# Optimization experiments

Hardware: AMD Instinct MI355X
Metric: run time of the kernel (lower is better)

Reference implementation:

```python
import jax, jax.numpy as jnp
import numpy as np

CHUNK = (10, 10, 10)          # chunk_shape from init_kwargs
VSHAPE = (40, 40, 200)        # spatial shape of each block
GRID_MAX = 1000               # locations drawn from [0, GRID_MAX)
SPAN = 256                    # > (GRID_MAX + max(VSHAPE)) / min(CHUNK); per-dim chunk-grid span for key linearization
NBATCH = 64


def setup_inputs() -> dict:
    key = jax.random.key(0)
    k1, k2 = jax.random.split(key)
    data = jax.random.normal(k1, (NBATCH, *VSHAPE), dtype=jnp.float32)
    location = jax.random.randint(k2, (NBATCH, 3), 0, GRID_MAX, dtype=jnp.int32)
    return {"data": data, "location": location}


def _chunkify(data, location):
    """Rebin each block into chunk-grid-aligned tiles of shape CHUNK.
    data: [B, V0, V1, V2]; location: [B, 3] int offsets in the global grid.
    Returns (chunks [M, *CHUNK], locs [M, 3]) with M = B * prod(nchunks)."""
    B = data.shape[0]
    C = jnp.array(CHUNK, dtype=jnp.int32)
    shift = location % C          # [B,3] offset of block origin within its first chunk
    start = location - shift      # [B,3] chunk-aligned envelope origin
    # Fixed-size envelope V + C per dim covers any shift in [0, C).
    E = tuple(v + c for v, c in zip(VSHAPE, CHUNK))
    nch = tuple(e // c for e, c in zip(E, CHUNK))  # chunks per dim: (5, 5, 21)

    def pad_one(d, sh):
        # padded[j0,j1,j2] = d[j - sh] where in range, else 0 (gather + mask, no scatter)
        idx = [jnp.arange(E[k]) - sh[k] for k in range(3)]
        valid = [(ix >= 0) & (ix < VSHAPE[k]) for k, ix in enumerate(idx)]
        cidx = [jnp.clip(ix, 0, VSHAPE[k] - 1) for k, ix in enumerate(idx)]
        g = d[cidx[0][:, None, None], cidx[1][None, :, None], cidx[2][None, None, :]]
        m = valid[0][:, None, None] & valid[1][None, :, None] & valid[2][None, None, :]
        return jnp.where(m, g, jnp.float32(0))

    padded = jax.vmap(pad_one)(data, shift)  # [B, E0, E1, E2]
    padded = padded.reshape(B, nch[0], CHUNK[0], nch[1], CHUNK[1], nch[2], CHUNK[2])
    chunks = padded.transpose(0, 1, 3, 5, 2, 4, 6).reshape(-1, *CHUNK)
    # per-chunk global locations
    g = jnp.stack(jnp.meshgrid(jnp.arange(nch[0]), jnp.arange(nch[1]),
                               jnp.arange(nch[2]), indexing='ij'), axis=-1)  # [n0,n1,n2,3]
    locs = start[:, None, None, None, :] + g[None].astype(jnp.int32) * C     # [B,n0,n1,n2,3]
    return chunks, locs.reshape(-1, 3)


def _accumulate(chunks, locs):
    """Sum chunks sharing the same global chunk location (scatter-add reduce).
    Output padded to a fixed M rows (jit-friendly); padding rows are zero."""
    M = chunks.shape[0]
    C = jnp.array(CHUNK, dtype=jnp.int32)
    cg = locs // C  # chunk-grid coordinates, each < SPAN
    keys = (cg[:, 0] * SPAN + cg[:, 1]) * SPAN + cg[:, 2]  # int32 linearized key
    ukeys, inv = jnp.unique(keys, return_inverse=True, size=M,
                            fill_value=jnp.int32(2**31 - 1))
    out = jax.ops.segment_sum(chunks.reshape(M, -1), inv, num_segments=M)
    out = out.reshape(M, *CHUNK)
    uloc = jnp.stack([ukeys // (SPAN * SPAN), (ukeys // SPAN) % SPAN,
                      ukeys % SPAN], axis=-1).astype(jnp.int32) * C
    return out, uloc


def reference(data, location):
    chunks, locs = _chunkify(data, location)
    return _accumulate(chunks, locs)
```

## Files before the change

### kernel.cpp

```cpp
#include <hip/hip_runtime.h>
#include <hip/hip_bf16.h>

namespace {
constexpr int NB    = 64;
constexpr int V0d   = 40, V1d = 40, V2d = 200;
constexpr int VOL   = V0d * V1d * V2d;
constexpr int NC0   = 5, NC1 = 5, NC2 = 21;
constexpr int CELLS = NC0 * NC1 * NC2;
constexpr int M     = NB * CELLS;
constexpr int C1MAX = 104, C2MAX = 120;
constexpr int KS    = 104 * C1MAX * C2MAX;
constexpr int SEG   = 4096;
constexpr int NSEG  = (KS + SEG - 1) / SEG;
constexpr int KSP   = NSEG * SEG;
constexpr int CHVOL = 1000;
}

__device__ __forceinline__ float bf16r(float v) {
    return __bfloat162float(__float2bfloat16(v));
}

__device__ __forceinline__ int enc(int c0, int c1, int c2) {
    return (c0 * C1MAX + c1) * C2MAX + c2;
}

__global__ void k_zero(int* __restrict__ P, int4* __restrict__ mask4) {
    int idx = blockIdx.x * blockDim.x + threadIdx.x;
    int stride = gridDim.x * blockDim.x;
    int4* p4 = reinterpret_cast<int4*>(P);
    const int n4 = KSP / 4;
    for (int i = idx; i < n4; i += stride) p4[i] = make_int4(0, 0, 0, 0);
    const int m4 = M * 8 / 16;
    for (int i = idx; i < m4; i += stride) mask4[i] = make_int4(0, 0, 0, 0);
}

__global__ void k_mark(const int* __restrict__ loc, int* __restrict__ P) {
    int m = blockIdx.x * blockDim.x + threadIdx.x;
    if (m >= M) return;
    int b = m / CELLS, cell = m % CELLS;
    int i = cell / (NC1 * NC2), j = (cell / NC2) % NC1, k = cell % NC2;
    P[enc(loc[b * 3 + 0] / 10 + i, loc[b * 3 + 1] / 10 + j,
          loc[b * 3 + 2] / 10 + k)] = 1;
}

__global__ __launch_bounds__(256) void k_scan_blocks(int* __restrict__ P,
                                                     int* __restrict__ Bsums) {
    int bid = blockIdx.x, t = threadIdx.x;
    int4* p4 = reinterpret_cast<int4*>(P + (size_t)bid * SEG + t * 16);
    int4 a = p4[0], b = p4[1], c = p4[2], d = p4[3];
    int v[16] = {a.x, a.y, a.z, a.w, b.x, b.y, b.z, b.w,
                 c.x, c.y, c.z, c.w, d.x, d.y, d.z, d.w};
    int s = 0;
#pragma unroll
    for (int e = 0; e < 16; ++e) s += v[e];
    __shared__ int sc[256];
    sc[t] = s;
    __syncthreads();
#pragma unroll
    for (int off = 1; off < 256; off <<= 1) {
        int x = (t >= off) ? sc[t - off] : 0;
        __syncthreads();
        sc[t] += x;
        __syncthreads();
    }
    int incl = sc[t];
    if (t == 255) Bsums[bid] = incl;
    int run = incl - s;
#pragma unroll
    for (int e = 0; e < 16; ++e) { int x = v[e]; v[e] = run; run += x; }
    p4[0] = make_int4(v[0], v[1], v[2], v[3]);
    p4[1] = make_int4(v[4], v[5], v[6], v[7]);
    p4[2] = make_int4(v[8], v[9], v[10], v[11]);
    p4[3] = make_int4(v[12], v[13], v[14], v[15]);
}

__global__ __launch_bounds__(256) void k_scan_sums(int* __restrict__ Bsums,
                                                   int* __restrict__ U) {
    __shared__ int sc[256];
    __shared__ int carry_s;
    int t = threadIdx.x;
    if (t == 0) carry_s = 0;
    __syncthreads();
    for (int base = 0; base < NSEG; base += 256) {
        int idx = base + t;
        int vv = (idx < NSEG) ? Bsums[idx] : 0;
        sc[t] = vv;
        __syncthreads();
#pragma unroll
        for (int off = 1; off < 256; off <<= 1) {
            int x = (t >= off) ? sc[t - off] : 0;
            __syncthreads();
            sc[t] += x;
            __syncthreads();
        }
        int incl = sc[t];
        int carry = carry_s;
        if (idx < NSEG) Bsums[idx] = carry + incl - vv;
        __syncthreads();
        if (t == 255) carry_s = carry + incl;
        __syncthreads();
    }
    if (t == 0) U[0] = carry_s;
}

__global__ void k_slots(const int* __restrict__ loc, const int* __restrict__ P,
                        const int* __restrict__ Bsums, int* __restrict__ ukeys,
                        unsigned long long* __restrict__ mask) {
    int m = blockIdx.x * blockDim.x + threadIdx.x;
    if (m >= M) return;
    int b = m / CELLS, cell = m % CELLS;
    int i = cell / (NC1 * NC2), j = (cell / NC2) % NC1, k = cell % NC2;
    int d = enc(loc[b * 3 + 0] / 10 + i, loc[b * 3 + 1] / 10 + j,
                loc[b * 3 + 2] / 10 + k);
    int rank = P[d] + Bsums[d / SEG];
    ukeys[rank] = d;
    atomicOr(&mask[rank], 1ull << b);
}

__global__ __launch_bounds__(256) void k_out(const float* __restrict__ data,
                                             const int* __restrict__ loc,
                                             const int* __restrict__ ukeys,
                                             const unsigned long long* __restrict__ mask,
                                             const int* __restrict__ U,
                                             float* __restrict__ out,
                                             long long base_ul) {
    int orig = blockIdx.x;
    int r = (orig & 7) * (M / 8) + (orig >> 3);
    int t = threadIdx.x;

    bool valid = (r < U[0]);
    float ax = 0.f, ay = 0.f, az = 0.f, aw = 0.f;
    int c0 = 0, c1 = 0, c2 = 0;

    if (valid) {
        int d = ukeys[r];
        c0 = d / (C1MAX * C2MAX);
        int rem = d % (C1MAX * C2MAX);
        c1 = rem / C2MAX;
        c2 = rem % C2MAX;
        if (t < 250) {
            int e0 = t * 4;
            int x  = e0 / 100;
            int rm = e0 % 100;
            int y  = rm / 10;
            int z0 = rm % 10;
            int g0 = c0 * 10, g1 = c1 * 10, g2 = c2 * 10;
            unsigned long long mk = mask[r];
            while (mk) {
                int b = __builtin_ctzll(mk);
                mk &= mk - 1;
                int l0 = loc[b * 3 + 0];
                int l1 = loc[b * 3 + 1];
                int l2 = loc[b * 3 + 2];
                const float* db = data + (size_t)b * VOL;
                if (z0 <= 6) {
                    int p0 = g0 - l0 + x, p1 = g1 - l1 + y, p2 = g2 - l2 + z0;
                    if ((unsigned)p0 < (unsigned)V0d &&
                        (unsigned)p1 < (unsigned)V1d) {
                        const float* s = db + (p0 * V1d + p1) * V2d + p2;
                        if (p2 >= 0 && p2 <= V2d - 4) {
                            ax += s[0]; ay += s[1]; az += s[2]; aw += s[3];
                        } else {
                            if ((unsigned)p2       < (unsigned)V2d) ax += s[0];
                            if ((unsigned)(p2 + 1) < (unsigned)V2d) ay += s[1];
                            if ((unsigned)(p2 + 2) < (unsigned)V2d) az += s[2];
                            if ((unsigned)(p2 + 3) < (unsigned)V2d) aw += s[3];
                        }
                    }
                } else {
                    float av[4] = {0.f, 0.f, 0.f, 0.f};
#pragma unroll
                    for (int j = 0; j < 4; ++j) {
                        int e  = e0 + j;
                        int xx = e / 100;
                        int rj = e % 100;
                        int yy = rj / 10, zz = rj % 10;
                        int q0 = g0 - l0 + xx, q1 = g1 - l1 + yy,
                            q2 = g2 - l2 + zz;
                        if ((unsigned)q0 < (unsigned)V0d &&
                            (unsigned)q1 < (unsigned)V1d &&
                            (unsigned)q2 < (unsigned)V2d)
                            av[j] = db[(q0 * V1d + q1) * V2d + q2];
                    }
                    ax += av[0]; ay += av[1]; az += av[2]; aw += av[3];
                }
            }
        }
    }

    if (t < 250) {
        *reinterpret_cast<float4*>(out + (long long)r * CHVOL + t * 4) =
            make_float4(bf16r(ax), bf16r(ay), bf16r(az), bf16r(aw));
    }
    if (t == 0) {
        float u0, u1, u2;
        if (valid) {
            u0 = (float)(c0 * 10);
            u1 = (float)(c1 * 10);
            u2 = (float)(c2 * 10);
        } else {
            u0 = 327670.f; u1 = 2550.f; u2 = 2550.f;
        }
        long long i = base_ul + (long long)r * 3;
        out[i + 0] = bf16r(u0);
        out[i + 1] = bf16r(u1);
        out[i + 2] = bf16r(u2);
    }
}

extern "C" void kernel_launch(void* const* d_in, const int* in_sizes, int n_in,
                              void* d_out, int out_size, void* d_ws, size_t ws_size,
                              hipStream_t stream) {
    const float* data = (const float*)d_in[0];
    const int* loc    = (const int*)d_in[1];
    float* out        = (float*)d_out;

    const size_t bytesP  = (size_t)KSP * 4;
    const size_t bytesSm = (size_t)M * 8
                         + (size_t)(NSEG + 64) * 4
                         + (size_t)M * 4 + 64;
    char* ws = (char*)d_ws;
    int* P;
    char* smalls;
    if (ws_size >= bytesP + bytesSm) {
        P      = (int*)ws;
        smalls = ws + bytesP;
    } else {
        P      = (int*)d_out;
        smalls = ws;
    }
    unsigned long long* mask = (unsigned long long*)smalls;
    int* Bsums = (int*)(smalls + (size_t)M * 8);
    int* ukeys = Bsums + NSEG + 64;
    int* U     = ukeys + M;

    long long out_sz  = (long long)out_size;
    long long base_ul = out_sz - (long long)3 * M;

    k_zero<<<640, 256, 0, stream>>>(P, (int4*)mask);
    k_mark<<<(M + 255) / 256, 256, 0, stream>>>(loc, P);
    k_scan_blocks<<<NSEG, 256, 0, stream>>>(P, Bsums);
    k_scan_sums<<<1, 256, 0, stream>>>(Bsums, U);
    k_slots<<<(M + 255) / 256, 256, 0, stream>>>(loc, P, Bsums, ukeys, mask);
    k_out<<<M, 256, 0, stream>>>(data, loc, ukeys, mask, U, out, base_ul);
}
```

Before: 63.76 us.

## Replace dense int presence array with bitset and popcount-based rank scan

The per-key int presence array (about 1.3M ints) becomes a 32-bit-word bitset marked with atomicOr. The scan now runs over per-word popcounts and ranks are computed with a masked popc, which cuts the zeroing and scan traffic roughly 32x. Validity in the output kernel now comes from a nonzero mask instead of a global unique count, and output stores are nontemporal. The remaining scan is only a few hundred entries, so launch overhead likely dominates those stages.

```diff
diff --git a/kernel.cpp b/kernel.cpp
--- a/kernel.cpp
+++ b/kernel.cpp
@@ -10,11 +10,13 @@
 constexpr int M     = NB * CELLS;
 constexpr int C1MAX = 104, C2MAX = 120;
 constexpr int KS    = 104 * C1MAX * C2MAX;
-constexpr int SEG   = 4096;
-constexpr int NSEG  = (KS + SEG - 1) / SEG;
-constexpr int KSP   = NSEG * SEG;
-constexpr int CHVOL = 1000;
-}
+constexpr int NWORDS = KS / 32;
+constexpr int NSB    = (NWORDS + 255) / 256;
+constexpr int NWPAD  = NSB * 256;
+constexpr int CHVOL  = 1000;
+}
+
+typedef float f32x4 __attribute__((ext_vector_type(4)));
 
 __device__ __forceinline__ float bf16r(float v) {
     return __bfloat162float(__float2bfloat16(v));
@@ -24,118 +26,95 @@
     return (c0 * C1MAX + c1) * C2MAX + c2;
 }
 
-__global__ void k_zero(int* __restrict__ P, int4* __restrict__ mask4) {
+__global__ void k_zero(int4* __restrict__ W4, int4* __restrict__ mask4) {
     int idx = blockIdx.x * blockDim.x + threadIdx.x;
     int stride = gridDim.x * blockDim.x;
-    int4* p4 = reinterpret_cast<int4*>(P);
-    const int n4 = KSP / 4;
-    for (int i = idx; i < n4; i += stride) p4[i] = make_int4(0, 0, 0, 0);
+    const int w4 = NWORDS / 4;
+    for (int i = idx; i < w4; i += stride) W4[i] = make_int4(0, 0, 0, 0);
     const int m4 = M * 8 / 16;
     for (int i = idx; i < m4; i += stride) mask4[i] = make_int4(0, 0, 0, 0);
 }
 
-__global__ void k_mark(const int* __restrict__ loc, int* __restrict__ P) {
-    int m = blockIdx.x * blockDim.x + threadIdx.x;
-    if (m >= M) return;
-    int b = m / CELLS, cell = m % CELLS;
-    int i = cell / (NC1 * NC2), j = (cell / NC2) % NC1, k = cell % NC2;
-    P[enc(loc[b * 3 + 0] / 10 + i, loc[b * 3 + 1] / 10 + j,
-          loc[b * 3 + 2] / 10 + k)] = 1;
-}
-
-__global__ __launch_bounds__(256) void k_scan_blocks(int* __restrict__ P,
-                                                     int* __restrict__ Bsums) {
-    int bid = blockIdx.x, t = threadIdx.x;
-    int4* p4 = reinterpret_cast<int4*>(P + (size_t)bid * SEG + t * 16);
-    int4 a = p4[0], b = p4[1], c = p4[2], d = p4[3];
-    int v[16] = {a.x, a.y, a.z, a.w, b.x, b.y, b.z, b.w,
-                 c.x, c.y, c.z, c.w, d.x, d.y, d.z, d.w};
-    int s = 0;
-#pragma unroll
-    for (int e = 0; e < 16; ++e) s += v[e];
-    __shared__ int sc[256];
-    sc[t] = s;
-    __syncthreads();
-#pragma unroll
-    for (int off = 1; off < 256; off <<= 1) {
-        int x = (t >= off) ? sc[t - off] : 0;
-        __syncthreads();
-        sc[t] += x;
-        __syncthreads();
-    }
-    int incl = sc[t];
-    if (t == 255) Bsums[bid] = incl;
-    int run = incl - s;
-#pragma unroll
-    for (int e = 0; e < 16; ++e) { int x = v[e]; v[e] = run; run += x; }
-    p4[0] = make_int4(v[0], v[1], v[2], v[3]);
-    p4[1] = make_int4(v[4], v[5], v[6], v[7]);
-    p4[2] = make_int4(v[8], v[9], v[10], v[11]);
-    p4[3] = make_int4(v[12], v[13], v[14], v[15]);
-}
-
-__global__ __launch_bounds__(256) void k_scan_sums(int* __restrict__ Bsums,
-                                                   int* __restrict__ U) {
-    __shared__ int sc[256];
-    __shared__ int carry_s;
-    int t = threadIdx.x;
-    if (t == 0) carry_s = 0;
-    __syncthreads();
-    for (int base = 0; base < NSEG; base += 256) {
-        int idx = base + t;
-        int vv = (idx < NSEG) ? Bsums[idx] : 0;
-        sc[t] = vv;
-        __syncthreads();
-#pragma unroll
-        for (int off = 1; off < 256; off <<= 1) {
-            int x = (t >= off) ? sc[t - off] : 0;
-            __syncthreads();
-            sc[t] += x;
-            __syncthreads();
-        }
-        int incl = sc[t];
-        int carry = carry_s;
-        if (idx < NSEG) Bsums[idx] = carry + incl - vv;
-        __syncthreads();
-        if (t == 255) carry_s = carry + incl;
-        __syncthreads();
-    }
-    if (t == 0) U[0] = carry_s;
-}
-
-__global__ void k_slots(const int* __restrict__ loc, const int* __restrict__ P,
-                        const int* __restrict__ Bsums, int* __restrict__ ukeys,
-                        unsigned long long* __restrict__ mask) {
+__global__ void k_mark(const int* __restrict__ loc, unsigned* __restrict__ W) {
     int m = blockIdx.x * blockDim.x + threadIdx.x;
     if (m >= M) return;
     int b = m / CELLS, cell = m % CELLS;
     int i = cell / (NC1 * NC2), j = (cell / NC2) % NC1, k = cell % NC2;
     int d = enc(loc[b * 3 + 0] / 10 + i, loc[b * 3 + 1] / 10 + j,
                 loc[b * 3 + 2] / 10 + k);
-    int rank = P[d] + Bsums[d / SEG];
+    atomicOr(&W[d >> 5], 1u << (d & 31));
+}
+
+__global__ __launch_bounds__(256) void k_scan_words(const unsigned* __restrict__ W,
+                                                    unsigned* __restrict__ WP,
+                                                    int* __restrict__ Bsums) {
+    int t = threadIdx.x;
+    int w = blockIdx.x * 256 + t;
+    int c = (w < NWORDS) ? __popc(W[w]) : 0;
+    __shared__ int sc[256];
+    sc[t] = c;
+    __syncthreads();
+#pragma unroll
+    for (int off = 1; off < 256; off <<= 1) {
+        int x = (t >= off) ? sc[t - off] : 0;
+        __syncthreads();
+        sc[t] += x;
+        __syncthreads();
+    }
+    int incl = sc[t];
+    WP[w] = (unsigned)(incl - c);
+    if (t == 255) Bsums[blockIdx.x] = incl;
+}
+
+__global__ __launch_bounds__(256) void k_scan_sums(int* __restrict__ Bsums) {
+    int t = threadIdx.x;
+    int vv = (t < NSB) ? Bsums[t] : 0;
+    __shared__ int sc[256];
+    sc[t] = vv;
+    __syncthreads();
+#pragma unroll
+    for (int off = 1; off < 256; off <<= 1) {
+        int x = (t >= off) ? sc[t - off] : 0;
+        __syncthreads();
+        sc[t] += x;
+        __syncthreads();
+    }
+    if (t < NSB) Bsums[t] = sc[t] - vv;
+}
+
+__global__ void k_slots(const int* __restrict__ loc, const unsigned* __restrict__ W,
+                        const unsigned* __restrict__ WP, const int* __restrict__ Bsums,
+                        int* __restrict__ ukeys, unsigned long long* __restrict__ mask) {
+    int m = blockIdx.x * blockDim.x + threadIdx.x;
+    if (m >= M) return;
+    int b = m / CELLS, cell = m % CELLS;
+    int i = cell / (NC1 * NC2), j = (cell / NC2) % NC1, k = cell % NC2;
+    int d = enc(loc[b * 3 + 0] / 10 + i, loc[b * 3 + 1] / 10 + j,
+                loc[b * 3 + 2] / 10 + k);
+    int w = d >> 5, bp = d & 31;
+    unsigned wd = W[w];
+    int rank = Bsums[w >> 8] + (int)WP[w] + __popc(wd & ((1u << bp) - 1u));
     ukeys[rank] = d;
     atomicOr(&mask[rank], 1ull << b);
 }
 
 __global__ __launch_bounds__(256) void k_out(const float* __restrict__ data,
-                                             const int* __restrict__ loc,
-                                             const int* __restrict__ ukeys,
-                                             const unsigned long long* __restrict__ mask,
-                                             const int* __restrict__ U,
-                                             float* __restrict__ out,
-                                             long long base_ul) {
+        const int* __restrict__ loc, const int* __restrict__ ukeys,
+        const unsigned long long* __restrict__ mask,
+        float* __restrict__ out, long long base_ul) {
     int orig = blockIdx.x;
     int r = (orig & 7) * (M / 8) + (orig >> 3);
     int t = threadIdx.x;
 
-    bool valid = (r < U[0]);
+    unsigned long long mk = mask[r];
+    int key = ukeys[r];
+    bool valid = (mk != 0ull);
+
     float ax = 0.f, ay = 0.f, az = 0.f, aw = 0.f;
     int c0 = 0, c1 = 0, c2 = 0;
-
     if (valid) {
-        int d = ukeys[r];
-        c0 = d / (C1MAX * C2MAX);
-        int rem = d % (C1MAX * C2MAX);
+        c0 = key / (C1MAX * C2MAX);
+        int rem = key % (C1MAX * C2MAX);
         c1 = rem / C2MAX;
         c2 = rem % C2MAX;
         if (t < 250) {
@@ -145,13 +124,11 @@
             int y  = rm / 10;
             int z0 = rm % 10;
             int g0 = c0 * 10, g1 = c1 * 10, g2 = c2 * 10;
-            unsigned long long mk = mask[r];
-            while (mk) {
-                int b = __builtin_ctzll(mk);
-                mk &= mk - 1;
-                int l0 = loc[b * 3 + 0];
-                int l1 = loc[b * 3 + 1];
-                int l2 = loc[b * 3 + 2];
+            unsigned long long m2 = mk;
+            while (m2) {
+                int b = __builtin_ctzll(m2);
+                m2 &= m2 - 1;
+                int l0 = loc[b * 3 + 0], l1 = loc[b * 3 + 1], l2 = loc[b * 3 + 2];
                 const float* db = data + (size_t)b * VOL;
                 if (z0 <= 6) {
                     int p0 = g0 - l0 + x, p1 = g1 - l1 + y, p2 = g2 - l2 + z0;
@@ -170,8 +147,8 @@
                 } else {
                     float av[4] = {0.f, 0.f, 0.f, 0.f};
 #pragma unroll
-                    for (int j = 0; j < 4; ++j) {
-                        int e  = e0 + j;
+                    for (int jj = 0; jj < 4; ++jj) {
+                        int e  = e0 + jj;
                         int xx = e / 100;
                         int rj = e % 100;
                         int yy = rj / 10, zz = rj % 10;
@@ -180,7 +157,7 @@
                         if ((unsigned)q0 < (unsigned)V0d &&
                             (unsigned)q1 < (unsigned)V1d &&
                             (unsigned)q2 < (unsigned)V2d)
-                            av[j] = db[(q0 * V1d + q1) * V2d + q2];
+                            av[jj] = db[(q0 * V1d + q1) * V2d + q2];
                     }
                     ax += av[0]; ay += av[1]; az += av[2]; aw += av[3];
                 }
@@ -189,8 +166,9 @@
     }
 
     if (t < 250) {
-        *reinterpret_cast<float4*>(out + (long long)r * CHVOL + t * 4) =
-            make_float4(bf16r(ax), bf16r(ay), bf16r(az), bf16r(aw));
+        f32x4 v = {bf16r(ax), bf16r(ay), bf16r(az), bf16r(aw)};
+        __builtin_nontemporal_store(v,
+            reinterpret_cast<f32x4*>(out + (long long)r * CHVOL + t * 4));
     }
     if (t == 0) {
         float u0, u1, u2;
@@ -202,9 +180,9 @@
             u0 = 327670.f; u1 = 2550.f; u2 = 2550.f;
         }
         long long i = base_ul + (long long)r * 3;
-        out[i + 0] = bf16r(u0);
-        out[i + 1] = bf16r(u1);
-        out[i + 2] = bf16r(u2);
+        __builtin_nontemporal_store(bf16r(u0), out + i + 0);
+        __builtin_nontemporal_store(bf16r(u1), out + i + 1);
+        __builtin_nontemporal_store(bf16r(u2), out + i + 2);
     }
 }
 
@@ -215,32 +193,28 @@
     const int* loc    = (const int*)d_in[1];
     float* out        = (float*)d_out;
 
-    const size_t bytesP  = (size_t)KSP * 4;
-    const size_t bytesSm = (size_t)M * 8
-                         + (size_t)(NSEG + 64) * 4
-                         + (size_t)M * 4 + 64;
-    char* ws = (char*)d_ws;
-    int* P;
-    char* smalls;
-    if (ws_size >= bytesP + bytesSm) {
-        P      = (int*)ws;
-        smalls = ws + bytesP;
-    } else {
-        P      = (int*)d_out;
-        smalls = ws;
-    }
-    unsigned long long* mask = (unsigned long long*)smalls;
-    int* Bsums = (int*)(smalls + (size_t)M * 8);
-    int* ukeys = Bsums + NSEG + 64;
-    int* U     = ukeys + M;
+    const size_t offMask  = 0;
+    const size_t offKeys  = offMask + (size_t)M * 8;
+    const size_t offW     = offKeys + (size_t)M * 4;
+    const size_t offWP    = offW + (size_t)NWPAD * 4;
+    const size_t offBs    = offWP + (size_t)NWPAD * 4;
+    const size_t bytesAll = offBs + (size_t)(NSB + 64) * 4;
+
+    char* basep = (ws_size >= bytesAll) ? (char*)d_ws : (char*)d_out;
+
+    unsigned long long* mask = (unsigned long long*)(basep + offMask);
+    int*      ukeys = (int*)(basep + offKeys);
+    unsigned* W     = (unsigned*)(basep + offW);
+    unsigned* WP    = (unsigned*)(basep + offWP);
+    int*      Bsums = (int*)(basep + offBs);
 
     long long out_sz  = (long long)out_size;
     long long base_ul = out_sz - (long long)3 * M;
 
-    k_zero<<<640, 256, 0, stream>>>(P, (int4*)mask);
-    k_mark<<<(M + 255) / 256, 256, 0, stream>>>(loc, P);
-    k_scan_blocks<<<NSEG, 256, 0, stream>>>(P, Bsums);
-    k_scan_sums<<<1, 256, 0, stream>>>(Bsums, U);
-    k_slots<<<(M + 255) / 256, 256, 0, stream>>>(loc, P, Bsums, ukeys, mask);
-    k_out<<<M, 256, 0, stream>>>(data, loc, ukeys, mask, U, out, base_ul);
-}
+    k_zero<<<128, 256, 0, stream>>>((int4*)W, (int4*)mask);
+    k_mark<<<(M + 255) / 256, 256, 0, stream>>>(loc, W);
+    k_scan_words<<<NSB, 256, 0, stream>>>(W, WP, Bsums);
+    k_scan_sums<<<1, 256, 0, stream>>>(Bsums);
+    k_slots<<<(M + 255) / 256, 256, 0, stream>>>(loc, W, WP, Bsums, ukeys, mask);
+    k_out<<<M, 256, 0, stream>>>(data, loc, ukeys, mask, out, base_ul);
+}
```

Result: faster. 60.85 us (-4.6%).
